# Optimization experiments

Hardware: AMD Instinct MI355X
Metric: run time of the kernel (lower is better)

The kernel has to match this reference:

```python
import jax, jax.numpy as jnp
import numpy as np

B, T = 64, 512
N_EMB, HIDDEN, VOCAB = 768, 256, 3072


def setup_inputs() -> dict:
    key = jax.random.key(0)
    ks = jax.random.split(key, 5)
    def xavier(k, shape):
        bound = float(np.sqrt(6.0 / (shape[0] + shape[1])))
        return jax.random.uniform(k, shape, jnp.float32, -bound, bound)
    return {
        "idx": jax.random.randint(ks[0], (B, T), 0, VOCAB),
        "emb_table": jax.random.normal(ks[1], (VOCAB, N_EMB), jnp.float32),
        "Wxh": xavier(ks[2], (N_EMB, HIDDEN)),
        "Whh": xavier(ks[3], (HIDDEN, HIDDEN)),
        "Wy": xavier(ks[4], (HIDDEN, VOCAB)),
        "By": jnp.zeros((VOCAB,), jnp.float32),
        "Bh": jnp.zeros((HIDDEN,), jnp.float32),
    }


def reference(idx, emb_table, Wxh, Whh, Wy, By, Bh):
    # embedded: [B, T, E] -> scan over time with hidden carry [B, H]
    embedded = emb_table[idx]                      # gather
    xWxh = jnp.einsum('bte,eh->tbh', embedded, Wxh)  # precompute input projection

    def step(hidden, x_t):
        hidden = jnp.tanh(x_t + hidden @ Whh + Bh)
        return hidden, None

    h0 = jnp.zeros((idx.shape[0], Whh.shape[0]), embedded.dtype)
    hidden, _ = jax.lax.scan(step, h0, xWxh)
    # return_sequences=False: only the last step's output is returned
    out = hidden @ Wy + By
    return out, hidden
```

## Files before the change

### kernel.cpp

```cpp
#include <hip/hip_runtime.h>
#include <hip/hip_bf16.h>

typedef _Float16 half8 __attribute__((ext_vector_type(8)));
typedef _Float16 half2_t __attribute__((ext_vector_type(2)));
typedef float f32x4 __attribute__((ext_vector_type(4)));

#define B_SZ 64
#define T_SZ 512
#define E_SZ 768
#define H_SZ 256
#define V_SZ 3072

#define WS_X     0u
#define WS_WT    16777216u
#define WS_WF    17170432u
#define WS_H     17301504u

static __device__ __forceinline__ float fast_tanh(float x) {
  float e = __builtin_amdgcn_exp2f(x * 2.8853900817779268f);
  return 1.0f - 2.0f * __builtin_amdgcn_rcpf(1.0f + e);
}

static __device__ __forceinline__ float dot2(unsigned int h2, unsigned int w2, float c) {
  return __builtin_amdgcn_fdot2(__builtin_bit_cast(half2_t, h2),
                                __builtin_bit_cast(half2_t, w2), c, false);
}

__global__ __launch_bounds__(256) void k0_convert(
    const float* __restrict__ Wxh,
    _Float16* __restrict__ Wt)
{
  int gid = blockIdx.x * 256 + threadIdx.x;
  if (gid < E_SZ * H_SZ) {
    int e = gid >> 8, h = gid & 255;
    Wt[h * E_SZ + e] = (_Float16)Wxh[gid];
  }
}

__global__ __launch_bounds__(256) void k1_xproj(
    const int* __restrict__ idx,
    const float* __restrict__ emb,
    const _Float16* __restrict__ Wt,
    _Float16* __restrict__ x)
{
  const int tid  = threadIdx.x;
  const int w    = tid >> 6;
  const int lane = tid & 63;
  const int m16  = lane & 15;
  const int quad = lane >> 4;
  const int r = blockIdx.x * 64 + w * 16 + m16;
  const int t = r >> 6;
  const int b = r & 63;
  const int erow = idx[b * T_SZ + t];
  const float* Arow = emb + (size_t)erow * E_SZ + quad * 8;

  __shared__ __align__(16) _Float16 bp[2][16 * 64 * 8];
  int n_[4], kb_[4];
#pragma unroll
  for (int pp = 0; pp < 4; ++pp) {
    int f = tid + 256 * pp;
    n_[pp]  = ((f >> 6) << 4) | (f & 15);
    kb_[pp] = (f >> 4) & 3;
  }
  uint4 stg[4];
#pragma unroll
  for (int pp = 0; pp < 4; ++pp)
    stg[pp] = *(const uint4*)(Wt + (size_t)n_[pp] * E_SZ + kb_[pp] * 8);
  f32x4 af0 = *(const f32x4*)(Arow);
  f32x4 af1 = *(const f32x4*)(Arow + 4);

  f32x4 acc[16];
#pragma unroll
  for (int n = 0; n < 16; ++n) { f32x4 z = {0.f, 0.f, 0.f, 0.f}; acc[n] = z; }

#pragma unroll
  for (int pp = 0; pp < 4; ++pp)
    *(uint4*)(bp[0] + (size_t)(tid + 256 * pp) * 8) = stg[pp];
  __syncthreads();

#pragma unroll 1
  for (int ki = 0; ki < 24; ++ki) {
    const _Float16* cur = bp[ki & 1];
    f32x4 af0n = af0, af1n = af1;
    if (ki < 23) {
#pragma unroll
      for (int pp = 0; pp < 4; ++pp)
        stg[pp] = *(const uint4*)(Wt + (size_t)n_[pp] * E_SZ + (ki + 1) * 32 + kb_[pp] * 8);
      af0n = *(const f32x4*)(Arow + (ki + 1) * 32);
      af1n = *(const f32x4*)(Arow + (ki + 1) * 32 + 4);
    }
    half8 a;
#pragma unroll
    for (int e = 0; e < 4; ++e) { a[e] = (_Float16)af0[e]; a[4 + e] = (_Float16)af1[e]; }
#pragma unroll
    for (int nt = 0; nt < 16; ++nt) {
      half8 bb = *(const half8*)(cur + (size_t)(nt * 64 + lane) * 8);
      acc[nt] = __builtin_amdgcn_mfma_f32_16x16x32_f16(a, bb, acc[nt], 0, 0, 0);
    }
    if (ki < 23) {
#pragma unroll
      for (int pp = 0; pp < 4; ++pp)
        *(uint4*)(bp[(ki + 1) & 1] + (size_t)(tid + 256 * pp) * 8) = stg[pp];
      __syncthreads();
    }
    af0 = af0n; af1 = af1n;
  }
  const int rbase = blockIdx.x * 64 + w * 16 + quad * 4;
#pragma unroll
  for (int nt = 0; nt < 16; ++nt) {
    const int col = nt * 16 + m16;
#pragma unroll
    for (int rg = 0; rg < 4; ++rg) {
      x[(size_t)(rbase + rg) * H_SZ + col] = (_Float16)acc[nt][rg];
    }
  }
}

__global__ __launch_bounds__(256, 1) void k2_rnn(
    const float* __restrict__ Whh,
    const _Float16* __restrict__ x,
    const float* __restrict__ Bh,
    float* __restrict__ hout,
    float* __restrict__ hidout)
{
  const int b   = blockIdx.x;
  const int tid = threadIdx.x;
  __shared__ __align__(16) _Float16 hb[2][H_SZ];

  unsigned int wc[128];
#pragma unroll
  for (int p = 0; p < 128; ++p) {
    _Float16 w0 = (_Float16)Whh[(size_t)(2 * p)     * H_SZ + tid];
    _Float16 w1 = (_Float16)Whh[(size_t)(2 * p + 1) * H_SZ + tid];
    half2_t pk; pk[0] = w0; pk[1] = w1;
    wc[p] = __builtin_bit_cast(unsigned int, pk);
  }

  const float bhj = Bh[tid];
  const _Float16* xp = x + b * H_SZ + tid;
  _Float16 xA = xp[0];
  _Float16 xB = xp[(size_t)(B_SZ * H_SZ)];
  hb[1][tid] = (_Float16)0.f;
  float hval = 0.f;
  __syncthreads();

#define RNN_STEP(HR, HW, XF)                                           \
  {                                                                    \
    const uint4* hq4 = (const uint4*)(HR);                             \
    float a0 = 0.f, a1 = 0.f, a2 = 0.f, a3 = 0.f;                      \
    _Pragma("unroll")                                                  \
    for (int kk = 0; kk < 32; ++kk) {                                  \
      uint4 hq = hq4[kk];                                              \
      a0 = dot2(hq.x, wc[4 * kk + 0], a0);                             \
      a1 = dot2(hq.y, wc[4 * kk + 1], a1);                             \
      a2 = dot2(hq.z, wc[4 * kk + 2], a2);                             \
      a3 = dot2(hq.w, wc[4 * kk + 3], a3);                             \
    }                                                                  \
    float y = (a0 + a1) + (a2 + a3);                                   \
    hval = fast_tanh(y + (XF));                                        \
    (HW)[tid] = (_Float16)hval;                                        \
    __syncthreads();                                                   \
  }

#pragma unroll 1
  for (int tt = 0; tt < 256; ++tt) {
    float xfA = (float)xA + bhj;
    int ta = 2 * tt + 2; ta = ta > 511 ? 511 : ta;
    xA = xp[(size_t)ta * (B_SZ * H_SZ)];
    RNN_STEP(hb[1], hb[0], xfA)
    float xfB = (float)xB + bhj;
    int tb = 2 * tt + 3; tb = tb > 511 ? 511 : tb;
    xB = xp[(size_t)tb * (B_SZ * H_SZ)];
    RNN_STEP(hb[0], hb[1], xfB)
  }
#undef RNN_STEP
  hout[b * H_SZ + tid] = hval;
  hidout[b * H_SZ + tid] = hval;
}

__global__ __launch_bounds__(256) void k3_out(
    const float* __restrict__ h,
    const float* __restrict__ Wy,
    const float* __restrict__ By,
    float* __restrict__ out)
{
  __shared__ float hs[H_SZ];
  const int c = blockIdx.x;
  const int b = blockIdx.y;
  const int v = c * 256 + threadIdx.x;
  hs[threadIdx.x] = h[b * H_SZ + threadIdx.x];
  __syncthreads();
  float acc = By[v];
#pragma unroll 8
  for (int jj = 0; jj < H_SZ; ++jj) {
    acc += hs[jj] * Wy[(size_t)jj * V_SZ + v];
  }
  out[(size_t)b * V_SZ + v] = acc;
}

extern "C" void kernel_launch(void* const* d_in, const int* in_sizes, int n_in,
                              void* d_out, int out_size, void* d_ws, size_t ws_size,
                              hipStream_t stream)
{
  const int*   idx = (const int*)d_in[0];
  const float* emb = (const float*)d_in[1];
  const float* Wxh = (const float*)d_in[2];
  const float* Whh = (const float*)d_in[3];
  const float* Wy  = (const float*)d_in[4];
  const float* By  = (const float*)d_in[5];
  const float* Bh  = (const float*)d_in[6];

  char* ws = (char*)d_ws;
  _Float16* x    = (_Float16*)(ws + WS_X);
  _Float16* Wt   = (_Float16*)(ws + WS_WT);
  float*    hbuf = (float*)(ws + WS_H);

  float* out    = (float*)d_out;
  float* hidout = out + (size_t)B_SZ * V_SZ;

  k0_convert<<<768, 256, 0, stream>>>(Wxh, Wt);
  k1_xproj  <<<512, 256, 0, stream>>>(idx, emb, Wt, x);
  k2_rnn    <<<64, 256, 0, stream>>>(Whh, x, Bh, hbuf, hidout);
  k3_out    <<<dim3(12, 64), 256, 0, stream>>>(hbuf, Wy, By, out);
}
```

Measured before the change: 443.6 us.

## Split RNN recurrence reduction across two thread groups with shared-memory partial sums

The recurrent kernel now uses 512 threads per batch row, with each half computing a partial dot product over 128 hidden inputs. The two partials are combined through shared memory before tanh. Whh is pre-packed into half2 pairs in the convert kernel, so the RNN kernel loads its register-resident weights directly. This halves the serial dot-product chain and the register weight footprint per step, at the cost of an extra barrier per timestep and an extra shared-memory exchange.

```diff
diff --git a/kernel.cpp b/kernel.cpp
--- a/kernel.cpp
+++ b/kernel.cpp
@@ -13,7 +13,7 @@
 
 #define WS_X     0u
 #define WS_WT    16777216u
-#define WS_WF    17170432u
+#define WS_WQ    17170432u
 #define WS_H     17301504u
 
 static __device__ __forceinline__ float fast_tanh(float x) {
@@ -28,12 +28,21 @@
 
 __global__ __launch_bounds__(256) void k0_convert(
     const float* __restrict__ Wxh,
-    _Float16* __restrict__ Wt)
+    const float* __restrict__ Whh,
+    _Float16* __restrict__ Wt,
+    unsigned int* __restrict__ Wq)
 {
   int gid = blockIdx.x * 256 + threadIdx.x;
   if (gid < E_SZ * H_SZ) {
     int e = gid >> 8, h = gid & 255;
     Wt[h * E_SZ + e] = (_Float16)Wxh[gid];
+  }
+  if (gid < 128 * H_SZ) {
+    int p = gid >> 8, c = gid & 255;
+    half2_t pk;
+    pk[0] = (_Float16)Whh[(size_t)(2 * p)     * H_SZ + c];
+    pk[1] = (_Float16)Whh[(size_t)(2 * p + 1) * H_SZ + c];
+    Wq[gid] = __builtin_bit_cast(unsigned int, pk);
   }
 }
 
@@ -116,8 +125,8 @@
   }
 }
 
-__global__ __launch_bounds__(256, 1) void k2_rnn(
-    const float* __restrict__ Whh,
+__global__ __launch_bounds__(512, 2) void k2_rnn(
+    const unsigned int* __restrict__ Wq,
     const _Float16* __restrict__ x,
     const float* __restrict__ Bh,
     float* __restrict__ hout,
@@ -125,57 +134,63 @@
 {
   const int b   = blockIdx.x;
   const int tid = threadIdx.x;
+  const int g   = tid >> 8;
+  const int c   = tid & 255;
   __shared__ __align__(16) _Float16 hb[2][H_SZ];
-
-  unsigned int wc[128];
-#pragma unroll
-  for (int p = 0; p < 128; ++p) {
-    _Float16 w0 = (_Float16)Whh[(size_t)(2 * p)     * H_SZ + tid];
-    _Float16 w1 = (_Float16)Whh[(size_t)(2 * p + 1) * H_SZ + tid];
-    half2_t pk; pk[0] = w0; pk[1] = w1;
-    wc[p] = __builtin_bit_cast(unsigned int, pk);
-  }
-
-  const float bhj = Bh[tid];
-  const _Float16* xp = x + b * H_SZ + tid;
+  __shared__ float part[H_SZ];
+
+  unsigned int wc[64];
+#pragma unroll
+  for (int i = 0; i < 64; ++i)
+    wc[i] = Wq[(size_t)(g * 64 + i) * H_SZ + c];
+
+  const float bhj = Bh[c];
+  const _Float16* xp = x + b * H_SZ + c;
   _Float16 xA = xp[0];
   _Float16 xB = xp[(size_t)(B_SZ * H_SZ)];
-  hb[1][tid] = (_Float16)0.f;
+  if (tid < H_SZ) hb[1][tid] = (_Float16)0.f;
   float hval = 0.f;
   __syncthreads();
 
-#define RNN_STEP(HR, HW, XF)                                           \
+#define K2_STEP(HR, HW, XREG)                                          \
   {                                                                    \
-    const uint4* hq4 = (const uint4*)(HR);                             \
+    const uint4* hq4 = ((const uint4*)(HR)) + g * 16;                  \
     float a0 = 0.f, a1 = 0.f, a2 = 0.f, a3 = 0.f;                      \
     _Pragma("unroll")                                                  \
-    for (int kk = 0; kk < 32; ++kk) {                                  \
+    for (int kk = 0; kk < 16; ++kk) {                                  \
       uint4 hq = hq4[kk];                                              \
       a0 = dot2(hq.x, wc[4 * kk + 0], a0);                             \
       a1 = dot2(hq.y, wc[4 * kk + 1], a1);                             \
       a2 = dot2(hq.z, wc[4 * kk + 2], a2);                             \
       a3 = dot2(hq.w, wc[4 * kk + 3], a3);                             \
     }                                                                  \
-    float y = (a0 + a1) + (a2 + a3);                                   \
-    hval = fast_tanh(y + (XF));                                        \
-    (HW)[tid] = (_Float16)hval;                                        \
+    float psum = (a0 + a1) + (a2 + a3);                                \
+    if (g) part[c] = psum;                                             \
+    __syncthreads();                                                   \
+    if (!g) {                                                          \
+      float y = psum + part[c] + (float)(XREG) + bhj;                  \
+      hval = fast_tanh(y);                                             \
+      (HW)[c] = (_Float16)hval;                                        \
+    }                                                                  \
     __syncthreads();                                                   \
   }
 
 #pragma unroll 1
   for (int tt = 0; tt < 256; ++tt) {
-    float xfA = (float)xA + bhj;
     int ta = 2 * tt + 2; ta = ta > 511 ? 511 : ta;
+    _Float16 xAc = xA;
     xA = xp[(size_t)ta * (B_SZ * H_SZ)];
-    RNN_STEP(hb[1], hb[0], xfA)
-    float xfB = (float)xB + bhj;
+    K2_STEP(hb[1], hb[0], xAc)
     int tb = 2 * tt + 3; tb = tb > 511 ? 511 : tb;
+    _Float16 xBc = xB;
     xB = xp[(size_t)tb * (B_SZ * H_SZ)];
-    RNN_STEP(hb[0], hb[1], xfB)
-  }
-#undef RNN_STEP
-  hout[b * H_SZ + tid] = hval;
-  hidout[b * H_SZ + tid] = hval;
+    K2_STEP(hb[0], hb[1], xBc)
+  }
+#undef K2_STEP
+  if (!g) {
+    hout[b * H_SZ + c] = hval;
+    hidout[b * H_SZ + c] = hval;
+  }
 }
 
 __global__ __launch_bounds__(256) void k3_out(
@@ -211,15 +226,16 @@
   const float* Bh  = (const float*)d_in[6];
 
   char* ws = (char*)d_ws;
-  _Float16* x    = (_Float16*)(ws + WS_X);
-  _Float16* Wt   = (_Float16*)(ws + WS_WT);
-  float*    hbuf = (float*)(ws + WS_H);
+  _Float16*     x    = (_Float16*)(ws + WS_X);
+  _Float16*     Wt   = (_Float16*)(ws + WS_WT);
+  unsigned int* Wq   = (unsigned int*)(ws + WS_WQ);
+  float*        hbuf = (float*)(ws + WS_H);
 
   float* out    = (float*)d_out;
   float* hidout = out + (size_t)B_SZ * V_SZ;
 
-  k0_convert<<<768, 256, 0, stream>>>(Wxh, Wt);
+  k0_convert<<<768, 256, 0, stream>>>(Wxh, Whh, Wt, Wq);
   k1_xproj  <<<512, 256, 0, stream>>>(idx, emb, Wt, x);
-  k2_rnn    <<<64, 256, 0, stream>>>(Whh, x, Bh, hbuf, hidout);
+  k2_rnn    <<<64, 512, 0, stream>>>(Wq, x, Bh, hbuf, hidout);
   k3_out    <<<dim3(12, 64), 256, 0, stream>>>(hbuf, Wy, By, out);
 }
```

Result: no change. 443.7 us (+0.0%).
